# Optimization experiments

Measured on AMD Instinct MI355X. Metric: run time of the kernel, lower is better.

## Reference

```python
import jax, jax.numpy as jnp
import numpy as np

N_NODES = 100000

def setup_inputs() -> dict:
    key = jax.random.key(0)
    k1, k2, k3, k4 = jax.random.split(key, 4)
    B, S, D, H = 50000, 10, 128, 128
    nodes = jax.random.randint(k1, (B,), 0, N_NODES, dtype=jnp.int64 if jax.config.jax_enable_x64 else jnp.int32)
    neigh_idx = jax.random.randint(k2, (B, S), 0, N_NODES, dtype=nodes.dtype)
    feature = jax.random.normal(k3, (N_NODES, D), dtype=jnp.float32)
    weight = jax.random.normal(k4, (2 * D, H), dtype=jnp.float32) * (1.0 / np.sqrt(2 * D))
    return {"nodes": nodes, "neigh_idx": neigh_idx, "feature": feature, "weight": weight}

def reference(nodes, neigh_idx, feature, weight):
    # Mean aggregation over sampled neighbors: [B, S, D] -> [B, D]
    neigh_feats = jnp.mean(feature[neigh_idx], axis=1)
    # Self features: [B, D]
    self_feats = feature[nodes]
    # Concat + linear + ReLU (gcn=False branch)
    combined = jnp.concatenate([self_feats, neigh_feats], axis=1)  # [B, 2D]
    return jax.nn.relu(combined @ weight)  # [B, H]
```

## Files before the change

kernel.cpp:

```cpp
#include <hip/hip_runtime.h>


typedef __attribute__((ext_vector_type(8))) short bf16x8;
typedef __attribute__((ext_vector_type(4))) float f32x4;

__device__ __forceinline__ unsigned short f2bf(float x) {
  unsigned int u = __float_as_uint(x);
  u += 0x7fffu + ((u >> 16) & 1u);
  return (unsigned short)(u >> 16);
}

__global__ void sage_prep_wt(const float* __restrict__ W,
                             unsigned short* __restrict__ Wt) {
  int tid = blockIdx.x * blockDim.x + threadIdx.x;
  float4 v = ((const float4*)W)[tid];
  int flat = tid << 2;
  int k = flat >> 7;
  int h = flat & 127;
  Wt[(h + 0) * 256 + k] = f2bf(v.x);
  Wt[(h + 1) * 256 + k] = f2bf(v.y);
  Wt[(h + 2) * 256 + k] = f2bf(v.z);
  Wt[(h + 3) * 256 + k] = f2bf(v.w);
}

__global__ __launch_bounds__(512, 6)
void sage_fused4(const int* __restrict__ nodes,
                 const int* __restrict__ neigh,
                 const float* __restrict__ feat,
                 const unsigned short* __restrict__ Wt,
                 float* __restrict__ out, int B)
{
  constexpr int K = 256, H = 128, S = 10;
  constexpr int TILE = 16;
  constexpr int STR = K + 8;
  __shared__ unsigned short Clds[TILE * STR];

  const int t = threadIdx.x;
  const int block0 = blockIdx.x * TILE;

  {
    const int r   = t >> 5;
    const int sub = t & 31;
    const int b   = block0 + r;
    unsigned short* crow = &Clds[r * STR];
    if (b < B) {
      const float4* f4 = (const float4*)feat;

      int nidx[S];
#pragma unroll
      for (int s = 0; s < S; ++s) nidx[s] = neigh[b * S + s];
      const long srow = (long)nodes[b] * 32;

      float4 self = f4[srow + sub];
      float4 v[S];
#pragma unroll
      for (int s = 0; s < S; ++s) v[s] = f4[(long)nidx[s] * 32 + sub];

      float ax = 0.f, ay = 0.f, az = 0.f, aw = 0.f;
#pragma unroll
      for (int s = 0; s < S; ++s) { ax += v[s].x; ay += v[s].y; az += v[s].z; aw += v[s].w; }

      ushort4 o;
      o.x = f2bf(self.x); o.y = f2bf(self.y); o.z = f2bf(self.z); o.w = f2bf(self.w);
      *(ushort4*)&crow[4 * sub] = o;
      o.x = f2bf(ax * 0.1f); o.y = f2bf(ay * 0.1f);
      o.z = f2bf(az * 0.1f); o.w = f2bf(aw * 0.1f);
      *(ushort4*)&crow[128 + 4 * sub] = o;
    } else {
      ushort4 z; z.x = z.y = z.z = z.w = 0;
      *(ushort4*)&crow[4 * sub] = z;
      *(ushort4*)&crow[128 + 4 * sub] = z;
    }
  }
  __syncthreads();
  __builtin_amdgcn_sched_barrier(0);

  const int lane = t & 63;
  const int wave = t >> 6;
  const int m    = lane & 15;
  const int quad = lane >> 4;
  const int cbase = wave * 16;

  bf16x8 bfrag[8];
#pragma unroll
  for (int ks = 0; ks < 8; ++ks)
    bfrag[ks] = *(const bf16x8*)&Wt[(cbase + m) * K + ks * 32 + quad * 8];

  f32x4 acc = {0.f, 0.f, 0.f, 0.f};
#pragma unroll
  for (int ks = 0; ks < 8; ++ks) {
    bf16x8 a = *(const bf16x8*)&Clds[m * STR + ks * 32 + quad * 8];
    acc = __builtin_amdgcn_mfma_f32_16x16x32_bf16(a, bfrag[ks], acc, 0, 0, 0);
  }

#pragma unroll
  for (int reg = 0; reg < 4; ++reg) {
    const int gb = block0 + quad * 4 + reg;
    if (gb < B) out[(size_t)gb * H + cbase + m] = fmaxf(acc[reg], 0.0f);
  }
}

extern "C" void kernel_launch(void* const* d_in, const int* in_sizes, int n_in,
                              void* d_out, int out_size, void* d_ws, size_t ws_size,
                              hipStream_t stream) {
  const int*   nodes = (const int*)d_in[0];
  const int*   neigh = (const int*)d_in[1];
  const float* feat  = (const float*)d_in[2];
  const float* W     = (const float*)d_in[3];
  float*       out   = (float*)d_out;
  const int B = in_sizes[0];

  unsigned short* Wt = (unsigned short*)d_ws;
  sage_prep_wt<<<32, 256, 0, stream>>>(W, Wt);
  const int grid = (B + 15) / 16;
  sage_fused4<<<grid, 512, 0, stream>>>(nodes, neigh, feat, Wt, out, B);
}
```

Baseline: 139.2 us.

## Stage neighbor feature gathers into LDS via global_load_lds in two passes

Replaces the per-thread register gather of 11 feature rows with direct global-to-LDS loads (global_load_lds), one wave per batch row, processed in two passes of 8 rows each. The staged rows are then reduced from LDS into the bf16 tile before the MFMA GEMM. The aim is to keep gather loads out of registers and issue more memory requests at once. In exchange it uses about 45KB more LDS per block, which limits occupancy, and adds two extra barriers per pass that serialize gather and reduce.

```diff
diff --git a/kernel.cpp b/kernel.cpp
--- a/kernel.cpp
+++ b/kernel.cpp
@@ -4,10 +4,16 @@
 typedef __attribute__((ext_vector_type(8))) short bf16x8;
 typedef __attribute__((ext_vector_type(4))) float f32x4;
 
+typedef __attribute__((address_space(1))) const float gfloat;
+typedef __attribute__((address_space(3))) float lfloat;
+
 __device__ __forceinline__ unsigned short f2bf(float x) {
   unsigned int u = __float_as_uint(x);
   u += 0x7fffu + ((u >> 16) & 1u);
   return (unsigned short)(u >> 16);
+}
+__device__ __forceinline__ unsigned int pack2bf(float lo, float hi) {
+  return (unsigned int)f2bf(lo) | ((unsigned int)f2bf(hi) << 16);
 }
 
 __global__ void sage_prep_wt(const float* __restrict__ W,
@@ -24,7 +30,7 @@
 }
 
 __global__ __launch_bounds__(512, 6)
-void sage_fused4(const int* __restrict__ nodes,
+void sage_fused5(const int* __restrict__ nodes,
                  const int* __restrict__ neigh,
                  const float* __restrict__ feat,
                  const unsigned short* __restrict__ Wt,
@@ -33,50 +39,59 @@
   constexpr int K = 256, H = 128, S = 10;
   constexpr int TILE = 16;
   constexpr int STR = K + 8;
-  __shared__ unsigned short Clds[TILE * STR];
+  __shared__ float stage[8 * 11 * 128];
+  __shared__ unsigned short tile[TILE * STR];
 
   const int t = threadIdx.x;
+  const int lane = t & 63;
+  const int wave = t >> 6;
   const int block0 = blockIdx.x * TILE;
 
-  {
-    const int r   = t >> 5;
-    const int sub = t & 31;
-    const int b   = block0 + r;
-    unsigned short* crow = &Clds[r * STR];
-    if (b < B) {
-      const float4* f4 = (const float4*)feat;
+  for (int p = 0; p < 2; ++p) {
+    {
+      int b = block0 + p * 8 + wave;
+      if (b >= B) b = B - 1;
+      int idx[11];
+      idx[0] = nodes[b];
+#pragma unroll
+      for (int s = 0; s < S; ++s) idx[s + 1] = neigh[(long)b * S + s];
 
-      int nidx[S];
+      const int stbase = wave * (11 * 128);
+      const int half = lane >> 5;
+      const int col4 = (lane & 31) * 4;
 #pragma unroll
-      for (int s = 0; s < S; ++s) nidx[s] = neigh[b * S + s];
-      const long srow = (long)nodes[b] * 32;
+      for (int j = 0; j < 5; ++j) {
+        int sidx = half ? idx[2 * j + 1] : idx[2 * j];
+        const float* g = feat + (long)sidx * 128 + col4;
+        lfloat* l = (lfloat*)&stage[stbase + j * 256];
+        __builtin_amdgcn_global_load_lds((gfloat*)g, l, 16, 0, 0);
+      }
+      if (lane < 32) {
+        const float* g = feat + (long)idx[10] * 128 + col4;
+        lfloat* l = (lfloat*)&stage[stbase + 5 * 256];
+        __builtin_amdgcn_global_load_lds((gfloat*)g, l, 16, 0, 0);
+      }
+    }
+    __syncthreads();
 
-      float4 self = f4[srow + sub];
-      float4 v[S];
+    {
+      const int stbase = wave * (11 * 128);
+      const int e2 = lane * 2;
+      float2 self = *(const float2*)&stage[stbase + e2];
+      float sx = 0.f, sy = 0.f;
 #pragma unroll
-      for (int s = 0; s < S; ++s) v[s] = f4[(long)nidx[s] * 32 + sub];
-
-      float ax = 0.f, ay = 0.f, az = 0.f, aw = 0.f;
-#pragma unroll
-      for (int s = 0; s < S; ++s) { ax += v[s].x; ay += v[s].y; az += v[s].z; aw += v[s].w; }
-
-      ushort4 o;
-      o.x = f2bf(self.x); o.y = f2bf(self.y); o.z = f2bf(self.z); o.w = f2bf(self.w);
-      *(ushort4*)&crow[4 * sub] = o;
-      o.x = f2bf(ax * 0.1f); o.y = f2bf(ay * 0.1f);
-      o.z = f2bf(az * 0.1f); o.w = f2bf(aw * 0.1f);
-      *(ushort4*)&crow[128 + 4 * sub] = o;
-    } else {
-      ushort4 z; z.x = z.y = z.z = z.w = 0;
-      *(ushort4*)&crow[4 * sub] = z;
-      *(ushort4*)&crow[128 + 4 * sub] = z;
+      for (int s = 1; s <= S; ++s) {
+        float2 v = *(const float2*)&stage[stbase + s * 128 + e2];
+        sx += v.x; sy += v.y;
+      }
+      unsigned short* crow = &tile[(p * 8 + wave) * STR];
+      *(unsigned int*)&crow[e2]       = pack2bf(self.x, self.y);
+      *(unsigned int*)&crow[128 + e2] = pack2bf(sx * 0.1f, sy * 0.1f);
     }
+    __syncthreads();
   }
-  __syncthreads();
   __builtin_amdgcn_sched_barrier(0);
 
-  const int lane = t & 63;
-  const int wave = t >> 6;
   const int m    = lane & 15;
   const int quad = lane >> 4;
   const int cbase = wave * 16;
@@ -89,7 +104,7 @@
   f32x4 acc = {0.f, 0.f, 0.f, 0.f};
 #pragma unroll
   for (int ks = 0; ks < 8; ++ks) {
-    bf16x8 a = *(const bf16x8*)&Clds[m * STR + ks * 32 + quad * 8];
+    bf16x8 a = *(const bf16x8*)&tile[m * STR + ks * 32 + quad * 8];
     acc = __builtin_amdgcn_mfma_f32_16x16x32_bf16(a, bfrag[ks], acc, 0, 0, 0);
   }
 
@@ -113,5 +128,5 @@
   unsigned short* Wt = (unsigned short*)d_ws;
   sage_prep_wt<<<32, 256, 0, stream>>>(W, Wt);
   const int grid = (B + 15) / 16;
-  sage_fused4<<<grid, 512, 0, stream>>>(nodes, neigh, feat, Wt, out, B);
+  sage_fused5<<<grid, 512, 0, stream>>>(nodes, neigh, feat, Wt, out, B);
 }
```

Result: slower. 168.2 us (+20.8%).
